# Performance work log

Hardware: AMD Instinct MI355X
Metric: run time of the kernel (lower is better)

The kernel has to match this reference:

```python
import jax, jax.numpy as jnp
import numpy as np

FLOOR = 1e-6  # PCEN floor offset
B, C, T = 128, 40, 8000


def setup_inputs() -> dict:
    key = jax.random.key(0)
    x = jax.random.uniform(key, (B, C, T), dtype=jnp.float32)  # non-negative energies
    alpha = jnp.full((C,), 0.96, dtype=jnp.float32)
    delta = jnp.full((C,), 2.0, dtype=jnp.float32)
    root = jnp.full((C,), 2.0, dtype=jnp.float32)
    ema_w = jnp.full((C,), 0.04, dtype=jnp.float32)  # per-channel smoothing coeff
    return {"x": x, "alpha": alpha, "delta": delta, "root": root, "ema_w": ema_w}


def _ema(x_tbc, w):
    # x_tbc: [T, B, C]; w: [C]. s_t = w*x_t + (1-w)*s_{t-1}, s_{-1} = x_0
    # (so s_0 = w*x_0 + (1-w)*x_0 = x_0, matching scan_torch's res[0] = x[0])
    def step(s, xi):
        s = w * xi + (1.0 - w) * s
        return s, s
    _, ema = jax.lax.scan(step, x_tbc[0], x_tbc)
    return ema  # [T, B, C]


def reference(x, alpha, delta, root, ema_w):
    # x: [B, C, T]
    w = jnp.clip(ema_w, 0.0, 1.0)
    xt = jnp.transpose(x, (2, 0, 1))                 # [T, B, C]
    ema = jnp.transpose(_ema(xt, w), (1, 2, 0))      # [B, C, T]
    a = jnp.minimum(alpha, 1.0)[:, None]             # [C, 1]
    one_over_r = 1.0 / jnp.maximum(root, 1.0)[:, None]
    d = delta[:, None]
    out = (x / (FLOOR + ema) ** a + d) ** one_over_r - d ** one_over_r
    return out  # [B, C, T]
```

## Files before the change

kernel.cpp:

```cpp
#include <hip/hip_runtime.h>
#include <math.h>

#define FLOOR_EPS 1e-6f
#define T_LEN 8000
#define C_CH 40
#define N_ROWS (128 * 40)
#define CHUNKS 4
#define CHUNK_LEN (T_LEN / CHUNKS)
#define NTILES 8
#define LOOKBACK 512
#define WAVES_PER_BLOCK 4

typedef float f32x4 __attribute__((ext_vector_type(4)));

__device__ __forceinline__ float fast_log2(float v) { return __builtin_amdgcn_logf(v); }
__device__ __forceinline__ float fast_exp2(float v) { return __builtin_amdgcn_exp2f(v); }
__device__ __forceinline__ float fast_sqrt(float v) { return __builtin_amdgcn_sqrtf(v); }

__global__ __launch_bounds__(256) void pcen_kernel(
    const float* __restrict__ x,
    const float* __restrict__ alpha,
    const float* __restrict__ delta,
    const float* __restrict__ root,
    const float* __restrict__ ema_w,
    float* __restrict__ out)
{
    const int wave  = threadIdx.x >> 6;
    const int lane  = threadIdx.x & 63;
    const int gid   = blockIdx.x * WAVES_PER_BLOCK + wave;
    const int row   = gid >> 2;
    const int chunk = gid & 3;
    if (row >= N_ROWS) return;
    const int c = row % C_CH;

    const float w     = fminf(fmaxf(ema_w[c], 0.0f), 1.0f);
    const float q     = 1.0f - w;
    const float a     = fminf(alpha[c], 1.0f);
    const float inv_r = 1.0f / fmaxf(root[c], 1.0f);
    const float d     = delta[c];
    const float d_pow = powf(d, inv_r);
    const bool  use_sqrt = (inv_r == 0.5f);

    float q4p[6];
    q4p[0] = (q * q) * (q * q);
    #pragma unroll
    for (int k = 1; k < 6; ++k) q4p[k] = q4p[k - 1] * q4p[k - 1];
    const float q256 = q4p[5] * q4p[5];

    float qp = 1.0f;
    #pragma unroll
    for (int k = 0; k < 6; ++k)
        if ((lane >> k) & 1) qp *= q4p[k];

    const int base  = row * T_LEN + chunk * CHUNK_LEN;
    const int vbase = base >> 2;

    float4 xv[NTILES];
    #pragma unroll
    for (int t = 0; t < NTILES; ++t) {
        const int  eidx   = t * 256 + lane * 4;
        const bool active = eidx < CHUNK_LEN;
        xv[t] = active ? ((const float4*)x)[vbase + t * 64 + lane]
                       : make_float4(0.f, 0.f, 0.f, 0.f);
    }

    float sc;
    if (chunk == 0) {
        sc = __shfl(xv[0].x, 0, 64);
    } else {
        float q8p[6];
        q8p[0] = q4p[0] * q4p[0];
        #pragma unroll
        for (int k = 1; k < 6; ++k) q8p[k] = q8p[k - 1] * q8p[k - 1];

        const float4* lp = (const float4*)(x + (size_t)row * T_LEN
                                           + chunk * CHUNK_LEN - LOOKBACK + lane * 8);
        float4 a0 = lp[0];
        float4 a1 = lp[1];
        float v = a0.x;
        v = fmaf(v, q, a0.y); v = fmaf(v, q, a0.z); v = fmaf(v, q, a0.w);
        v = fmaf(v, q, a1.x); v = fmaf(v, q, a1.y); v = fmaf(v, q, a1.z); v = fmaf(v, q, a1.w);
        float S = w * v;
        const int m = 63 - lane;
        float scale = 1.0f;
        #pragma unroll
        for (int k = 0; k < 6; ++k)
            if ((m >> k) & 1) scale *= q8p[k];
        S *= scale;
        #pragma unroll
        for (int k = 0; k < 6; ++k)
            S += __shfl_xor(S, 1 << k, 64);
        sc = S;
    }

    float B[NTILES];
    #pragma unroll
    for (int t = 0; t < NTILES; ++t) {
        float b = xv[t].x;
        b = fmaf(b, q, xv[t].y);
        b = fmaf(b, q, xv[t].z);
        b = fmaf(b, q, xv[t].w);
        B[t] = w * b;
    }

    #pragma unroll
    for (int k = 0; k < 6; ++k) {
        float Bp[NTILES];
        #pragma unroll
        for (int t = 0; t < NTILES; ++t) Bp[t] = __shfl_up(B[t], 1u << k, 64);
        #pragma unroll
        for (int t = 0; t < NTILES; ++t)
            if (lane >= (1 << k)) B[t] = fmaf(q4p[k], Bp[t], B[t]);
    }

    float Blast[NTILES];
    #pragma unroll
    for (int t = 0; t < NTILES; ++t) Blast[t] = __shfl(B[t], 63, 64);

    #pragma unroll
    for (int t = 0; t < NTILES; ++t) {
        float Bexcl = __shfl_up(B[t], 1, 64);
        if (lane == 0) Bexcl = 0.0f;

        float s  = fmaf(qp, sc, Bexcl);
        float e0 = fmaf(q, s,  w * xv[t].x);
        float e1 = fmaf(q, e0, w * xv[t].y);
        float e2 = fmaf(q, e1, w * xv[t].z);
        float e3 = fmaf(q, e2, w * xv[t].w);

        float y0 = fmaf(xv[t].x, fast_exp2(-a * fast_log2(FLOOR_EPS + e0)), d);
        float y1 = fmaf(xv[t].y, fast_exp2(-a * fast_log2(FLOOR_EPS + e1)), d);
        float y2 = fmaf(xv[t].z, fast_exp2(-a * fast_log2(FLOOR_EPS + e2)), d);
        float y3 = fmaf(xv[t].w, fast_exp2(-a * fast_log2(FLOOR_EPS + e3)), d);

        f32x4 ov;
        if (use_sqrt) {
            ov.x = fast_sqrt(y0) - d_pow;
            ov.y = fast_sqrt(y1) - d_pow;
            ov.z = fast_sqrt(y2) - d_pow;
            ov.w = fast_sqrt(y3) - d_pow;
        } else {
            ov.x = fast_exp2(inv_r * fast_log2(y0)) - d_pow;
            ov.y = fast_exp2(inv_r * fast_log2(y1)) - d_pow;
            ov.z = fast_exp2(inv_r * fast_log2(y2)) - d_pow;
            ov.w = fast_exp2(inv_r * fast_log2(y3)) - d_pow;
        }

        const int eidx = t * 256 + lane * 4;
        if (eidx < CHUNK_LEN)
            __builtin_nontemporal_store(ov, &((f32x4*)out)[vbase + t * 64 + lane]);

        sc = fmaf(q256, sc, Blast[t]);
    }
}

extern "C" void kernel_launch(void* const* d_in, const int* in_sizes, int n_in,
                              void* d_out, int out_size, void* d_ws, size_t ws_size,
                              hipStream_t stream) {
    const float* x     = (const float*)d_in[0];
    const float* alpha = (const float*)d_in[1];
    const float* delta = (const float*)d_in[2];
    const float* root  = (const float*)d_in[3];
    const float* ema_w = (const float*)d_in[4];
    float* out = (float*)d_out;

    const int total_waves = N_ROWS * CHUNKS;
    const int grid = (total_waves + WAVES_PER_BLOCK - 1) / WAVES_PER_BLOCK;
    pcen_kernel<<<grid, 256, 0, stream>>>(x, alpha, delta, root, ema_w, out);
}
```

Measured before the change: 56.38 us.

## Give each lane 8 contiguous elements per tile and derive exclusive prefix algebraically

Each lane now owns 8 consecutive samples per tile instead of 4, which halves the number of tiles and therefore the cross-lane shuffle scan steps over the chunk. The exclusive prefix is recovered as (inclusive minus own) times 1/q^8 rather than through an extra shuffle. The cost is a longer serial recurrence per lane and a division by q^8, which can lose precision or hit denormals when q is small. Global accesses become two float4 per lane with a 32-byte stride between lanes, which may reduce coalescing efficiency.

```diff
diff --git a/kernel.cpp b/kernel.cpp
--- a/kernel.cpp
+++ b/kernel.cpp
@@ -7,7 +7,7 @@
 #define N_ROWS (128 * 40)
 #define CHUNKS 4
 #define CHUNK_LEN (T_LEN / CHUNKS)
-#define NTILES 8
+#define NTILES 4
 #define LOOKBACK 512
 #define WAVES_PER_BLOCK 4
 
@@ -41,40 +41,38 @@
     const float d_pow = powf(d, inv_r);
     const bool  use_sqrt = (inv_r == 0.5f);
 
-    float q4p[6];
-    q4p[0] = (q * q) * (q * q);
+    const float q2 = q * q, q4 = q2 * q2;
+    float q8p[6];
+    q8p[0] = q4 * q4;
     #pragma unroll
-    for (int k = 1; k < 6; ++k) q4p[k] = q4p[k - 1] * q4p[k - 1];
-    const float q256 = q4p[5] * q4p[5];
+    for (int k = 1; k < 6; ++k) q8p[k] = q8p[k - 1] * q8p[k - 1];
+    const float q512   = q8p[5] * q8p[5];
+    const float inv_q8 = (q8p[0] > 0.0f) ? 1.0f / q8p[0] : 0.0f;
 
     float qp = 1.0f;
     #pragma unroll
     for (int k = 0; k < 6; ++k)
-        if ((lane >> k) & 1) qp *= q4p[k];
+        if ((lane >> k) & 1) qp *= q8p[k];
 
-    const int base  = row * T_LEN + chunk * CHUNK_LEN;
-    const int vbase = base >> 2;
+    const int base = row * T_LEN + chunk * CHUNK_LEN;
 
-    float4 xv[NTILES];
+    float4 xa[NTILES], xb[NTILES];
     #pragma unroll
     for (int t = 0; t < NTILES; ++t) {
-        const int  eidx   = t * 256 + lane * 4;
-        const bool active = eidx < CHUNK_LEN;
-        xv[t] = active ? ((const float4*)x)[vbase + t * 64 + lane]
-                       : make_float4(0.f, 0.f, 0.f, 0.f);
+        const bool active = (t * 512 + lane * 8) < CHUNK_LEN;
+        const float4* xp = (const float4*)(x + (size_t)base) + t * 128 + lane * 2;
+        if (active) { xa[t] = xp[0]; xb[t] = xp[1]; }
+        else {
+            xa[t] = make_float4(0.f, 0.f, 0.f, 0.f);
+            xb[t] = make_float4(0.f, 0.f, 0.f, 0.f);
+        }
     }
 
     float sc;
     if (chunk == 0) {
-        sc = __shfl(xv[0].x, 0, 64);
+        sc = __shfl(xa[0].x, 0, 64);
     } else {
-        float q8p[6];
-        q8p[0] = q4p[0] * q4p[0];
-        #pragma unroll
-        for (int k = 1; k < 6; ++k) q8p[k] = q8p[k - 1] * q8p[k - 1];
-
-        const float4* lp = (const float4*)(x + (size_t)row * T_LEN
-                                           + chunk * CHUNK_LEN - LOOKBACK + lane * 8);
+        const float4* lp = (const float4*)(x + (size_t)base - LOOKBACK + lane * 8);
         float4 a0 = lp[0];
         float4 a1 = lp[1];
         float v = a0.x;
@@ -93,14 +91,19 @@
         sc = S;
     }
 
-    float B[NTILES];
+    float Bown[NTILES], B[NTILES];
     #pragma unroll
     for (int t = 0; t < NTILES; ++t) {
-        float b = xv[t].x;
-        b = fmaf(b, q, xv[t].y);
-        b = fmaf(b, q, xv[t].z);
-        b = fmaf(b, q, xv[t].w);
-        B[t] = w * b;
+        float b = xa[t].x;
+        b = fmaf(b, q, xa[t].y);
+        b = fmaf(b, q, xa[t].z);
+        b = fmaf(b, q, xa[t].w);
+        b = fmaf(b, q, xb[t].x);
+        b = fmaf(b, q, xb[t].y);
+        b = fmaf(b, q, xb[t].z);
+        b = fmaf(b, q, xb[t].w);
+        Bown[t] = w * b;
+        B[t] = Bown[t];
     }
 
     #pragma unroll
@@ -110,7 +113,7 @@
         for (int t = 0; t < NTILES; ++t) Bp[t] = __shfl_up(B[t], 1u << k, 64);
         #pragma unroll
         for (int t = 0; t < NTILES; ++t)
-            if (lane >= (1 << k)) B[t] = fmaf(q4p[k], Bp[t], B[t]);
+            if (lane >= (1 << k)) B[t] = fmaf(q8p[k], Bp[t], B[t]);
     }
 
     float Blast[NTILES];
@@ -119,38 +122,50 @@
 
     #pragma unroll
     for (int t = 0; t < NTILES; ++t) {
-        float Bexcl = __shfl_up(B[t], 1, 64);
-        if (lane == 0) Bexcl = 0.0f;
+        const float Bexcl = (B[t] - Bown[t]) * inv_q8;
+        float e = fmaf(qp, sc, Bexcl);
 
-        float s  = fmaf(qp, sc, Bexcl);
-        float e0 = fmaf(q, s,  w * xv[t].x);
-        float e1 = fmaf(q, e0, w * xv[t].y);
-        float e2 = fmaf(q, e1, w * xv[t].z);
-        float e3 = fmaf(q, e2, w * xv[t].w);
+        float ee[8];
+        e = fmaf(q, e,  w * xa[t].x); ee[0] = e;
+        e = fmaf(q, e,  w * xa[t].y); ee[1] = e;
+        e = fmaf(q, e,  w * xa[t].z); ee[2] = e;
+        e = fmaf(q, e,  w * xa[t].w); ee[3] = e;
+        e = fmaf(q, e,  w * xb[t].x); ee[4] = e;
+        e = fmaf(q, e,  w * xb[t].y); ee[5] = e;
+        e = fmaf(q, e,  w * xb[t].z); ee[6] = e;
+        e = fmaf(q, e,  w * xb[t].w); ee[7] = e;
 
-        float y0 = fmaf(xv[t].x, fast_exp2(-a * fast_log2(FLOOR_EPS + e0)), d);
-        float y1 = fmaf(xv[t].y, fast_exp2(-a * fast_log2(FLOOR_EPS + e1)), d);
-        float y2 = fmaf(xv[t].z, fast_exp2(-a * fast_log2(FLOOR_EPS + e2)), d);
-        float y3 = fmaf(xv[t].w, fast_exp2(-a * fast_log2(FLOOR_EPS + e3)), d);
+        const float xs[8] = { xa[t].x, xa[t].y, xa[t].z, xa[t].w,
+                              xb[t].x, xb[t].y, xb[t].z, xb[t].w };
+        float yy[8];
+        #pragma unroll
+        for (int j = 0; j < 8; ++j)
+            yy[j] = fmaf(xs[j], fast_exp2(-a * fast_log2(FLOOR_EPS + ee[j])), d);
 
-        f32x4 ov;
+        f32x4 o0, o1;
         if (use_sqrt) {
-            ov.x = fast_sqrt(y0) - d_pow;
-            ov.y = fast_sqrt(y1) - d_pow;
-            ov.z = fast_sqrt(y2) - d_pow;
-            ov.w = fast_sqrt(y3) - d_pow;
+            o0.x = fast_sqrt(yy[0]) - d_pow; o0.y = fast_sqrt(yy[1]) - d_pow;
+            o0.z = fast_sqrt(yy[2]) - d_pow; o0.w = fast_sqrt(yy[3]) - d_pow;
+            o1.x = fast_sqrt(yy[4]) - d_pow; o1.y = fast_sqrt(yy[5]) - d_pow;
+            o1.z = fast_sqrt(yy[6]) - d_pow; o1.w = fast_sqrt(yy[7]) - d_pow;
         } else {
-            ov.x = fast_exp2(inv_r * fast_log2(y0)) - d_pow;
-            ov.y = fast_exp2(inv_r * fast_log2(y1)) - d_pow;
-            ov.z = fast_exp2(inv_r * fast_log2(y2)) - d_pow;
-            ov.w = fast_exp2(inv_r * fast_log2(y3)) - d_pow;
+            o0.x = fast_exp2(inv_r * fast_log2(yy[0])) - d_pow;
+            o0.y = fast_exp2(inv_r * fast_log2(yy[1])) - d_pow;
+            o0.z = fast_exp2(inv_r * fast_log2(yy[2])) - d_pow;
+            o0.w = fast_exp2(inv_r * fast_log2(yy[3])) - d_pow;
+            o1.x = fast_exp2(inv_r * fast_log2(yy[4])) - d_pow;
+            o1.y = fast_exp2(inv_r * fast_log2(yy[5])) - d_pow;
+            o1.z = fast_exp2(inv_r * fast_log2(yy[6])) - d_pow;
+            o1.w = fast_exp2(inv_r * fast_log2(yy[7])) - d_pow;
         }
 
-        const int eidx = t * 256 + lane * 4;
-        if (eidx < CHUNK_LEN)
-            __builtin_nontemporal_store(ov, &((f32x4*)out)[vbase + t * 64 + lane]);
+        if ((t * 512 + lane * 8) < CHUNK_LEN) {
+            f32x4* op = (f32x4*)(out + (size_t)base) + t * 128 + lane * 2;
+            __builtin_nontemporal_store(o0, op);
+            __builtin_nontemporal_store(o1, op + 1);
+        }
 
-        sc = fmaf(q256, sc, Blast[t]);
+        sc = fmaf(q512, sc, Blast[t]);
     }
 }
 
```

Result: slower. 68.04 us (+20.7%).
